# Kernel tuning notes

Hardware: AMD Instinct MI355X
Metric: run time of the kernel (lower is better)

Reference implementation:

```python
import jax, jax.numpy as jnp
import numpy as np

EPS = 1e-12  # F.normalize eps
NUM_CLASSES = 80


def _l2_normalize(x, axis):
    # matches torch F.normalize: x / max(||x||_2, eps)
    n = jnp.sqrt(jnp.sum(x * x, axis=axis, keepdims=True))
    return x / jnp.maximum(n, EPS)


def setup_inputs() -> dict:
    key = jax.random.key(0)
    k1, k2, k3, k4 = jax.random.split(key, 4)
    B, C, H, W = 16, 256, 128, 128
    N = NUM_CLASSES
    features = jax.random.normal(k1, (B, C, H, W), dtype=jnp.float32)
    centroids = jax.random.normal(k2, (N, C), dtype=jnp.float32)
    fc_w = jax.random.normal(k3, (C, C, 1, 1), dtype=jnp.float32) * 0.02
    fc_b = jax.random.normal(k4, (C,), dtype=jnp.float32) * 0.01
    return {"features": features, "centroids": centroids, "fc_w": fc_w, "fc_b": fc_b}


def reference(features, centroids, fc_w, fc_b):
    N = centroids.shape[0]
    # cosine similarity to class centroids: [B, N, H, W]
    sim = jnp.einsum('bchw,nc->bnhw', _l2_normalize(features, axis=1),
                     _l2_normalize(centroids, axis=1))
    # hard one-hot assignment along class dim (scatter of argmax)
    idx = jnp.argmax(sim, axis=1)                              # [B, H, W]
    mask = jax.nn.one_hot(idx, N, axis=1, dtype=features.dtype)  # [B, N, H, W]
    # per-image, per-class mean feature (gather/blend)
    sum_x = jnp.einsum('bnhw,bchw->bnc', mask, features)       # [B, N, C]
    count = jnp.sum(mask, axis=(2, 3))[:, :, None]             # [B, N, 1]
    cent = sum_x / jnp.maximum(count, 1.0)
    delta = jnp.einsum('bnhw,bnc->bchw', mask, cent) - features
    alpha = jnp.exp(-jnp.mean(jnp.square(delta), axis=1, keepdims=True))  # [B,1,H,W]
    x = features + alpha * delta
    # 1x1 conv == channel matmul
    out = jnp.einsum('bchw,oc->bohw', x, fc_w[:, :, 0, 0]) + fc_b[None, :, None, None]
    return jax.nn.relu(out)
```

## Files before the change

### kernel.cpp

```cpp
#include <hip/hip_runtime.h>


typedef __bf16 bf16x8 __attribute__((ext_vector_type(8)));
typedef float  f32x4  __attribute__((ext_vector_type(4)));
typedef unsigned char u8;

__device__ __forceinline__ unsigned short f2b(float f) {
  unsigned u = __float_as_uint(f);
  return (unsigned short)((u + 0x7fffu + ((u >> 16) & 1u)) >> 16);
}
__device__ __forceinline__ float b2f(unsigned short s) {
  return __uint_as_float((unsigned)s << 16);
}

__global__ __launch_bounds__(256) void k0_cnorm(const float* __restrict__ cent,
                                                float* __restrict__ cnT) {
  int n = blockIdx.x, t = threadIdx.x;
  float v = cent[n * 256 + t];
  float s = v * v;
  #pragma unroll
  for (int o = 32; o > 0; o >>= 1) s += __shfl_down(s, o, 64);
  __shared__ float red[4];
  if ((t & 63) == 0) red[t >> 6] = s;
  __syncthreads();
  float tot = red[0] + red[1] + red[2] + red[3];
  float dn = fmaxf(sqrtf(tot), 1e-12f);
  cnT[t * 80 + n] = v / dn;
}

__global__ __launch_bounds__(256) void k0_wprep(const float* __restrict__ fcw,
                                                unsigned short* __restrict__ wks,
                                                float* __restrict__ wt) {
  int o = blockIdx.x, c = threadIdx.x;
  float w = fcw[o * 256 + c];
  wt[c * 256 + o] = w;
  wks[((c >> 5) * 256 + o) * 32 + (c & 31)] = f2b(w);
}

__global__ __launch_bounds__(256) void k1_argmax(const float* __restrict__ feat,
                                                 const float* __restrict__ cnT,
                                                 u8* __restrict__ idxb,
                                                 float* __restrict__ fsqg,
                                                 int* __restrict__ cntg) {
  __shared__ int lh[80];
  int t = threadIdx.x;
  if (t < 80) lh[t] = 0;
  __syncthreads();
  int b = blockIdx.x >> 6;
  int pi = ((blockIdx.x & 63) << 8) | t;
  const float* fb = feat + (size_t)b * 256 * 16384 + pi;
  float g[80];
  #pragma unroll
  for (int n = 0; n < 80; ++n) g[n] = 0.f;
  float fsq = 0.f;
  #pragma unroll 4
  for (int c = 0; c < 256; ++c) {
    float v = fb[(size_t)c * 16384];
    fsq = fmaf(v, v, fsq);
    const float* cr = cnT + c * 80;
    #pragma unroll
    for (int n = 0; n < 80; ++n) g[n] = fmaf(v, cr[n], g[n]);
  }
  float best = g[0]; int bi = 0;
  #pragma unroll
  for (int n = 1; n < 80; ++n) if (g[n] > best) { best = g[n]; bi = n; }
  idxb[b * 16384 + pi] = (u8)bi;
  fsqg[b * 16384 + pi] = fsq;
  atomicAdd(&lh[bi], 1);
  __syncthreads();
  if (t < 80) atomicAdd(&cntg[b * 80 + t], lh[t]);
}

__global__ __launch_bounds__(256) void k1b_gemm(const float* __restrict__ feat,
                                                const u8* __restrict__ idxb,
                                                unsigned short* __restrict__ sumxp) {
  int bid = blockIdx.x;
  int kp = bid & 3, ns = (bid >> 2) & 7, b = bid >> 5;
  int t = threadIdx.x, wv = t >> 6, ln = t & 63, lo = ln & 15, hi = ln >> 4;
  int nt = wv & 1;
  int m0 = (wv >> 1) ? 3 : 0, nm = (wv >> 1) ? 2 : 3;
  int c = ns * 32 + nt * 16 + lo;
  const float* fp = feat + (((size_t)b * 256 + c) * 16384 + kp * 4096 + hi * 8);
  const u8* ip = idxb + b * 16384 + kp * 4096 + hi * 8;
  f32x4 acc[3];
  f32x4 zz = {0.f, 0.f, 0.f, 0.f};
  acc[0] = zz; acc[1] = zz; acc[2] = zz;
  for (int ks = 0; ks < 128; ++ks) {
    float4 v0 = *(const float4*)(fp + ks * 32);
    float4 v1 = *(const float4*)(fp + ks * 32 + 4);
    union { unsigned short u[8]; bf16x8 v; } bb;
    bb.u[0] = f2b(v0.x); bb.u[1] = f2b(v0.y); bb.u[2] = f2b(v0.z); bb.u[3] = f2b(v0.w);
    bb.u[4] = f2b(v1.x); bb.u[5] = f2b(v1.y); bb.u[6] = f2b(v1.z); bb.u[7] = f2b(v1.w);
    uint2 iv = *(const uint2*)(ip + ks * 32);
    int id[8];
    #pragma unroll
    for (int j = 0; j < 4; ++j) { id[j] = (iv.x >> (8 * j)) & 255; id[4 + j] = (iv.y >> (8 * j)) & 255; }
    #pragma unroll
    for (int mi = 0; mi < 3; ++mi) {
      if (mi >= nm) break;
      int row = (m0 + mi) * 16 + lo;
      union { unsigned short u[8]; bf16x8 v; } ma;
      #pragma unroll
      for (int j = 0; j < 8; ++j) ma.u[j] = (id[j] == row) ? (unsigned short)0x3F80 : (unsigned short)0;
      acc[mi] = __builtin_amdgcn_mfma_f32_16x16x32_bf16(ma.v, bb.v, acc[mi], 0, 0, 0);
    }
  }
  #pragma unroll
  for (int mi = 0; mi < 3; ++mi) {
    if (mi >= nm) break;
    #pragma unroll
    for (int r = 0; r < 4; ++r) {
      int cls = (m0 + mi) * 16 + hi * 4 + r;
      sumxp[(((size_t)kp * 16 + b) * 80 + cls) * 256 + ns * 32 + nt * 16 + lo] = f2b(acc[mi][r]);
    }
  }
}

__global__ __launch_bounds__(256) void k2_cent(const unsigned short* __restrict__ sumxp,
                                               const int* __restrict__ cntg,
                                               const float* __restrict__ wt,
                                               unsigned short* __restrict__ centf,
                                               float* __restrict__ csqg,
                                               float* __restrict__ chatg) {
  int bn = blockIdx.x; int t = threadIdx.x;
  float dn = fmaxf((float)cntg[bn], 1.0f);
  float s = 0.f;
  #pragma unroll
  for (int kp = 0; kp < 4; ++kp)
    s += b2f(sumxp[((size_t)kp * 1280 + bn) * 256 + t]);
  float cv = s / dn;
  __shared__ float cl[256];
  __shared__ float red[4];
  cl[t] = cv;
  centf[(size_t)bn * 256 + t] = f2b(cv);
  float q = cv * cv;
  #pragma unroll
  for (int o = 32; o > 0; o >>= 1) q += __shfl_down(q, o, 64);
  if ((t & 63) == 0) red[t >> 6] = q;
  __syncthreads();
  if (t == 0) csqg[bn] = red[0] + red[1] + red[2] + red[3];
  float acc = 0.f;
  #pragma unroll 4
  for (int c = 0; c < 256; ++c) acc = fmaf(wt[c * 256 + t], cl[c], acc);
  chatg[(size_t)bn * 256 + t] = acc;
}

__global__ __launch_bounds__(256) void k3a_alpha(const float* __restrict__ feat,
                                                 const u8* __restrict__ idxb,
                                                 const float* __restrict__ csqg,
                                                 const unsigned short* __restrict__ centf,
                                                 float* __restrict__ fsq_alpha) {
  int b = blockIdx.x >> 6;
  int pi = ((blockIdx.x & 63) << 8) | threadIdx.x;
  const float* fb = feat + (size_t)b * 256 * 16384 + pi;
  int idx = idxb[b * 16384 + pi];
  const unsigned short* cw = centf + ((size_t)b * 80 + idx) * 256;
  float sel = 0.f;
  #pragma unroll 4
  for (int c = 0; c < 256; c += 8) {
    uint4 cc = *(const uint4*)&cw[c];
    float v0 = fb[(size_t)(c + 0) * 16384];
    float v1 = fb[(size_t)(c + 1) * 16384];
    float v2 = fb[(size_t)(c + 2) * 16384];
    float v3 = fb[(size_t)(c + 3) * 16384];
    float v4 = fb[(size_t)(c + 4) * 16384];
    float v5 = fb[(size_t)(c + 5) * 16384];
    float v6 = fb[(size_t)(c + 6) * 16384];
    float v7 = fb[(size_t)(c + 7) * 16384];
    sel = fmaf(v0, b2f((unsigned short)(cc.x & 0xffff)), sel);
    sel = fmaf(v1, b2f((unsigned short)(cc.x >> 16)), sel);
    sel = fmaf(v2, b2f((unsigned short)(cc.y & 0xffff)), sel);
    sel = fmaf(v3, b2f((unsigned short)(cc.y >> 16)), sel);
    sel = fmaf(v4, b2f((unsigned short)(cc.z & 0xffff)), sel);
    sel = fmaf(v5, b2f((unsigned short)(cc.z >> 16)), sel);
    sel = fmaf(v6, b2f((unsigned short)(cc.w & 0xffff)), sel);
    sel = fmaf(v7, b2f((unsigned short)(cc.w >> 16)), sel);
  }
  float fsq = fsq_alpha[b * 16384 + pi];
  float msq = (csqg[b * 80 + idx] - 2.f * sel + fsq) * (1.f / 256.f);
  fsq_alpha[b * 16384 + pi] = expf(-msq);
}

__global__ __launch_bounds__(512) void k3b_gemm(const float* __restrict__ feat,
    const u8* __restrict__ idxb, const float* __restrict__ alphag,
    const float* __restrict__ chatg, const unsigned short* __restrict__ wks,
    const float* __restrict__ fcb, float* __restrict__ out) {
  __shared__ alignas(16) unsigned short featT[64 * 264];
  const int t = threadIdx.x;
  const int w = t >> 6, ln = t & 63, lo = ln & 15, hi = ln >> 4;

  bf16x8 wf[2][8];
  #pragma unroll
  for (int ml = 0; ml < 2; ++ml)
    #pragma unroll
    for (int ks = 0; ks < 8; ++ks)
      wf[ml][ks] = *(const bf16x8*)&wks[((size_t)ks * 256 + (w * 2 + ml) * 16 + lo) * 32 + hi * 8];
  f32x4 bias2[2];
  #pragma unroll
  for (int ml = 0; ml < 2; ++ml)
    bias2[ml] = *(const f32x4*)&fcb[w * 32 + ml * 16 + hi * 4];

  for (int rep = 0; rep < 2; ++rep) {
    int tile = blockIdx.x * 2 + rep;
    int b = tile >> 8;
    int p0 = (tile & 255) << 6;

    {
      int pl = t & 63, cph = t >> 6;
      const float* fb = feat + ((size_t)b * 256 + cph * 32) * 16384 + p0 + pl;
      #pragma unroll
      for (int jj = 0; jj < 4; ++jj) {
        union { unsigned short u[8]; uint4 q; } pk;
        #pragma unroll
        for (int e = 0; e < 8; ++e) pk.u[e] = f2b(fb[(size_t)(jj * 8 + e) * 16384]);
        *(uint4*)&featT[pl * 264 + cph * 32 + jj * 8] = pk.q;
      }
    }
    __syncthreads();

    f32x4 acc[2][4];
    f32x4 zz = {0.f, 0.f, 0.f, 0.f};
    #pragma unroll
    for (int ml = 0; ml < 2; ++ml)
      #pragma unroll
      for (int pt = 0; pt < 4; ++pt) acc[ml][pt] = zz;

    #pragma unroll
    for (int ks = 0; ks < 8; ++ks) {
      bf16x8 bfr[4];
      #pragma unroll
      for (int pt = 0; pt < 4; ++pt)
        bfr[pt] = *(const bf16x8*)&featT[(pt * 16 + lo) * 264 + ks * 32 + hi * 8];
      #pragma unroll
      for (int ml = 0; ml < 2; ++ml)
        #pragma unroll
        for (int pt = 0; pt < 4; ++pt)
          acc[ml][pt] = __builtin_amdgcn_mfma_f32_16x16x32_bf16(wf[ml][ks], bfr[pt], acc[ml][pt], 0, 0, 0);
    }

    #pragma unroll
    for (int pt = 0; pt < 4; ++pt) {
      int p = p0 + pt * 16 + lo;
      float a = alphag[(size_t)b * 16384 + p];
      float om = 1.f - a;
      int cid = idxb[b * 16384 + p];
      const float* crow = chatg + ((size_t)b * 80 + cid) * 256;
      #pragma unroll
      for (int ml = 0; ml < 2; ++ml) {
        int o0 = w * 32 + ml * 16 + hi * 4;
        float4 c4 = *(const float4*)&crow[o0];
        size_t ob = ((size_t)b * 256 + o0) * 16384 + p;
        out[ob            ] = fmaxf(fmaf(a, c4.x, om * acc[ml][pt][0]) + bias2[ml][0], 0.f);
        out[ob + 16384    ] = fmaxf(fmaf(a, c4.y, om * acc[ml][pt][1]) + bias2[ml][1], 0.f);
        out[ob + 2 * 16384] = fmaxf(fmaf(a, c4.z, om * acc[ml][pt][2]) + bias2[ml][2], 0.f);
        out[ob + 3 * 16384] = fmaxf(fmaf(a, c4.w, om * acc[ml][pt][3]) + bias2[ml][3], 0.f);
      }
    }
    __syncthreads();
  }
}

extern "C" void kernel_launch(void* const* d_in, const int* in_sizes, int n_in,
                              void* d_out, int out_size, void* d_ws, size_t ws_size,
                              hipStream_t stream) {
  (void)in_sizes; (void)n_in; (void)out_size; (void)ws_size;
  const float* feat = (const float*)d_in[0];
  const float* cent = (const float*)d_in[1];
  const float* fcw  = (const float*)d_in[2];
  const float* fcb  = (const float*)d_in[3];
  float* out = (float*)d_out;
  char* ws = (char*)d_ws;
  float* cnT             = (float*)(ws);
  float* wt              = (float*)(ws + 81920);
  unsigned short* wks    = (unsigned short*)(ws + 344064);
  unsigned short* centf  = (unsigned short*)(ws + 475136);
  u8*    idxb            = (u8*)(ws + 1130496);
  float* fsq_alpha       = (float*)(ws + 1392640);
  int*   cntg            = (int*)(ws + 2441216);
  float* csq             = (float*)(ws + 2446336);
  float* chat            = (float*)(ws + 2451456);
  unsigned short* sumxp  = (unsigned short*)(ws + 3762176);

  hipMemsetAsync(cntg, 0, 16 * 80 * sizeof(int), stream);
  k0_cnorm<<<80, 256, 0, stream>>>(cent, cnT);
  k0_wprep<<<256, 256, 0, stream>>>(fcw, wks, wt);
  k1_argmax<<<1024, 256, 0, stream>>>(feat, cnT, idxb, fsq_alpha, cntg);
  k1b_gemm<<<512, 256, 0, stream>>>(feat, idxb, sumxp);
  k2_cent<<<1280, 256, 0, stream>>>(sumxp, cntg, wt, centf, csq, chat);
  k3a_alpha<<<1024, 256, 0, stream>>>(feat, idxb, csq, centf, fsq_alpha);
  k3b_gemm<<<2048, 512, 0, stream>>>(feat, idxb, fsq_alpha, chat, wks, fcb, out);
}
```

Measured before the change: 482.5 us.

## Fuse alpha computation into output GEMM and fold count memset into centroid kernel

Removes the separate alpha kernel, which reread the whole feature tensor from global memory. The GEMM kernel now computes each pixel's alpha from the bf16 feature tile it already holds in shared memory, using eight lanes per pixel and a shuffle reduction, and stores it in a small shared array. The per-class count zeroing moves from a hipMemsetAsync call into the centroid-normalization kernel, saving one launch. The cost is an extra barrier per tile and computing the selected-centroid dot product from bf16-rounded features rather than fp32, which slightly changes alpha.

```diff
diff --git a/kernel.cpp b/kernel.cpp
--- a/kernel.cpp
+++ b/kernel.cpp
@@ -14,8 +14,10 @@
 }
 
 __global__ __launch_bounds__(256) void k0_cnorm(const float* __restrict__ cent,
-                                                float* __restrict__ cnT) {
+                                                float* __restrict__ cnT,
+                                                int* __restrict__ cntg) {
   int n = blockIdx.x, t = threadIdx.x;
+  if (t < 16) cntg[n * 16 + t] = 0;
   float v = cent[n * 256 + t];
   float s = v * v;
   #pragma unroll
@@ -145,47 +147,13 @@
   chatg[(size_t)bn * 256 + t] = acc;
 }
 
-__global__ __launch_bounds__(256) void k3a_alpha(const float* __restrict__ feat,
-                                                 const u8* __restrict__ idxb,
-                                                 const float* __restrict__ csqg,
-                                                 const unsigned short* __restrict__ centf,
-                                                 float* __restrict__ fsq_alpha) {
-  int b = blockIdx.x >> 6;
-  int pi = ((blockIdx.x & 63) << 8) | threadIdx.x;
-  const float* fb = feat + (size_t)b * 256 * 16384 + pi;
-  int idx = idxb[b * 16384 + pi];
-  const unsigned short* cw = centf + ((size_t)b * 80 + idx) * 256;
-  float sel = 0.f;
-  #pragma unroll 4
-  for (int c = 0; c < 256; c += 8) {
-    uint4 cc = *(const uint4*)&cw[c];
-    float v0 = fb[(size_t)(c + 0) * 16384];
-    float v1 = fb[(size_t)(c + 1) * 16384];
-    float v2 = fb[(size_t)(c + 2) * 16384];
-    float v3 = fb[(size_t)(c + 3) * 16384];
-    float v4 = fb[(size_t)(c + 4) * 16384];
-    float v5 = fb[(size_t)(c + 5) * 16384];
-    float v6 = fb[(size_t)(c + 6) * 16384];
-    float v7 = fb[(size_t)(c + 7) * 16384];
-    sel = fmaf(v0, b2f((unsigned short)(cc.x & 0xffff)), sel);
-    sel = fmaf(v1, b2f((unsigned short)(cc.x >> 16)), sel);
-    sel = fmaf(v2, b2f((unsigned short)(cc.y & 0xffff)), sel);
-    sel = fmaf(v3, b2f((unsigned short)(cc.y >> 16)), sel);
-    sel = fmaf(v4, b2f((unsigned short)(cc.z & 0xffff)), sel);
-    sel = fmaf(v5, b2f((unsigned short)(cc.z >> 16)), sel);
-    sel = fmaf(v6, b2f((unsigned short)(cc.w & 0xffff)), sel);
-    sel = fmaf(v7, b2f((unsigned short)(cc.w >> 16)), sel);
-  }
-  float fsq = fsq_alpha[b * 16384 + pi];
-  float msq = (csqg[b * 80 + idx] - 2.f * sel + fsq) * (1.f / 256.f);
-  fsq_alpha[b * 16384 + pi] = expf(-msq);
-}
-
 __global__ __launch_bounds__(512) void k3b_gemm(const float* __restrict__ feat,
-    const u8* __restrict__ idxb, const float* __restrict__ alphag,
+    const u8* __restrict__ idxb, const float* __restrict__ fsqg,
+    const float* __restrict__ csqg, const unsigned short* __restrict__ centf,
     const float* __restrict__ chatg, const unsigned short* __restrict__ wks,
     const float* __restrict__ fcb, float* __restrict__ out) {
   __shared__ alignas(16) unsigned short featT[64 * 264];
+  __shared__ float alphal[64];
   const int t = threadIdx.x;
   const int w = t >> 6, ln = t & 63, lo = ln & 15, hi = ln >> 4;
 
@@ -218,6 +186,35 @@
     }
     __syncthreads();
 
+    {
+      int p = t >> 3, sub = t & 7;
+      int cid = idxb[b * 16384 + p0 + p];
+      const unsigned short* cw = centf + ((size_t)b * 80 + cid) * 256 + sub * 32;
+      const unsigned short* fr = &featT[p * 264 + sub * 32];
+      float sel = 0.f;
+      #pragma unroll
+      for (int j = 0; j < 4; ++j) {
+        uint4 cc = *(const uint4*)&cw[j * 8];
+        uint4 ff = *(const uint4*)&fr[j * 8];
+        sel = fmaf(b2f((unsigned short)(ff.x & 0xffff)), b2f((unsigned short)(cc.x & 0xffff)), sel);
+        sel = fmaf(b2f((unsigned short)(ff.x >> 16)),    b2f((unsigned short)(cc.x >> 16)),    sel);
+        sel = fmaf(b2f((unsigned short)(ff.y & 0xffff)), b2f((unsigned short)(cc.y & 0xffff)), sel);
+        sel = fmaf(b2f((unsigned short)(ff.y >> 16)),    b2f((unsigned short)(cc.y >> 16)),    sel);
+        sel = fmaf(b2f((unsigned short)(ff.z & 0xffff)), b2f((unsigned short)(cc.z & 0xffff)), sel);
+        sel = fmaf(b2f((unsigned short)(ff.z >> 16)),    b2f((unsigned short)(cc.z >> 16)),    sel);
+        sel = fmaf(b2f((unsigned short)(ff.w & 0xffff)), b2f((unsigned short)(cc.w & 0xffff)), sel);
+        sel = fmaf(b2f((unsigned short)(ff.w >> 16)),    b2f((unsigned short)(cc.w >> 16)),    sel);
+      }
+      sel += __shfl_xor(sel, 1, 64);
+      sel += __shfl_xor(sel, 2, 64);
+      sel += __shfl_xor(sel, 4, 64);
+      if (sub == 0) {
+        float fsq = fsqg[b * 16384 + p0 + p];
+        float msq = (csqg[b * 80 + cid] - 2.f * sel + fsq) * (1.f / 256.f);
+        alphal[p] = expf(-msq);
+      }
+    }
+
     f32x4 acc[2][4];
     f32x4 zz = {0.f, 0.f, 0.f, 0.f};
     #pragma unroll
@@ -237,11 +234,13 @@
         for (int pt = 0; pt < 4; ++pt)
           acc[ml][pt] = __builtin_amdgcn_mfma_f32_16x16x32_bf16(wf[ml][ks], bfr[pt], acc[ml][pt], 0, 0, 0);
     }
+    __syncthreads();
 
     #pragma unroll
     for (int pt = 0; pt < 4; ++pt) {
-      int p = p0 + pt * 16 + lo;
-      float a = alphag[(size_t)b * 16384 + p];
+      int pl = pt * 16 + lo;
+      int p = p0 + pl;
+      float a = alphal[pl];
       float om = 1.f - a;
       int cid = idxb[b * 16384 + p];
       const float* crow = chatg + ((size_t)b * 80 + cid) * 256;
@@ -275,18 +274,16 @@
   unsigned short* wks    = (unsigned short*)(ws + 344064);
   unsigned short* centf  = (unsigned short*)(ws + 475136);
   u8*    idxb            = (u8*)(ws + 1130496);
-  float* fsq_alpha       = (float*)(ws + 1392640);
+  float* fsq             = (float*)(ws + 1392640);
   int*   cntg            = (int*)(ws + 2441216);
   float* csq             = (float*)(ws + 2446336);
   float* chat            = (float*)(ws + 2451456);
   unsigned short* sumxp  = (unsigned short*)(ws + 3762176);
 
-  hipMemsetAsync(cntg, 0, 16 * 80 * sizeof(int), stream);
-  k0_cnorm<<<80, 256, 0, stream>>>(cent, cnT);
+  k0_cnorm<<<80, 256, 0, stream>>>(cent, cnT, cntg);
   k0_wprep<<<256, 256, 0, stream>>>(fcw, wks, wt);
-  k1_argmax<<<1024, 256, 0, stream>>>(feat, cnT, idxb, fsq_alpha, cntg);
+  k1_argmax<<<1024, 256, 0, stream>>>(feat, cnT, idxb, fsq, cntg);
   k1b_gemm<<<512, 256, 0, stream>>>(feat, idxb, sumxp);
   k2_cent<<<1280, 256, 0, stream>>>(sumxp, cntg, wt, centf, csq, chat);
-  k3a_alpha<<<1024, 256, 0, stream>>>(feat, idxb, csq, centf, fsq_alpha);
-  k3b_gemm<<<2048, 512, 0, stream>>>(feat, idxb, fsq_alpha, chat, wks, fcb, out);
-}
+  k3b_gemm<<<2048, 512, 0, stream>>>(feat, idxb, fsq, csq, centf, chat, wks, fcb, out);
+}
```

Result: faster. 465.6 us (-3.5%).
